# Kernel optimization log

Hardware: AMD Instinct MI355X
Metric: run time of the kernel (lower is better)

## Reference

```python
import jax, jax.numpy as jnp
import numpy as np
from jax.ops import segment_sum

N_NODES = 100000
N_EDGES = 1600000
IN_DIM, HID_DIM, OUT_DIM = 64, 48, 32


def setup_inputs() -> dict:
    key = jax.random.key(0)
    ks = jax.random.split(key, 4)
    x = jax.random.normal(ks[0], (N_NODES, IN_DIM), dtype=jnp.float32)
    edge_index = jax.random.randint(ks[1], (2, N_EDGES), 0, N_NODES, dtype=jnp.int64)
    W1 = jax.random.normal(ks[2], (IN_DIM, HID_DIM), dtype=jnp.float32) / np.sqrt(IN_DIM)
    b1 = jnp.zeros((HID_DIM,), dtype=jnp.float32)
    W2 = jax.random.normal(ks[3], (HID_DIM, OUT_DIM), dtype=jnp.float32) / np.sqrt(HID_DIM)
    b2 = jnp.zeros((OUT_DIM,), dtype=jnp.float32)
    return {"x": x, "edge_index": edge_index, "W1": W1, "b1": b1, "W2": W2, "b2": b2}


def _gcn_conv(x, W, b, src, dst, deg_inv_sqrt, n_nodes):
    # GCNConv: out = D^{-1/2} (A + I) D^{-1/2} (x W) + b
    h = x @ W                                   # [N, F_out]
    norm = deg_inv_sqrt[src] * deg_inv_sqrt[dst]  # [E+N]
    msg = h[src] * norm[:, None]                # gather + scale
    out = segment_sum(msg, dst, num_segments=n_nodes)  # scatter-add over dst
    return out + b


def reference(x, edge_index, W1, b1, W2, b2):
    n = x.shape[0]
    loop = jnp.arange(n, dtype=edge_index.dtype)
    src = jnp.concatenate([edge_index[0], loop])  # add self-loops (PyG default)
    dst = jnp.concatenate([edge_index[1], loop])
    deg = segment_sum(jnp.ones_like(dst, dtype=x.dtype), dst, num_segments=n)
    deg_inv_sqrt = jnp.where(deg > 0, jax.lax.rsqrt(jnp.maximum(deg, 1.0)), 0.0)
    h = _gcn_conv(x, W1, b1, src, dst, deg_inv_sqrt, n)
    h = jax.nn.relu(h)
    embeddings = _gcn_conv(h, W2, b2, src, dst, deg_inv_sqrt, n)
    return embeddings
```

## Files before the change

kernel.cpp:

```cpp
#include <hip/hip_runtime.h>
#include <hip/hip_fp16.h>


#define NN 100000
#define NE 1600000
#define NPB 128
#define NBUCK ((NN + NPB - 1) / NPB)
#define PBITS 17
#define PMASK ((1 << PBITS) - 1)
#define CHB 3
#define CHS 14
#define NKEY (NPB << CHB)
#define CAP 4096
#define UN 8
#define PART_B 512
#define EPT 8
#define RUNW (PART_B * EPT)
#define PART_G ((NE + RUNW - 1) / RUNW)
#define GROWS 256
#define GEMM_G ((NN + GROWS - 1) / GROWS)
#define GB NBUCK

struct alignas(8)  half4 { __half2 lo, hi; };
struct alignas(16) half8 { __half2 a, b, c, d; };

__global__ __launch_bounds__(512) void
k_lsortgemm(const int* __restrict__ src, const int* __restrict__ dst,
            int* __restrict__ runs, unsigned int* __restrict__ seg,
            const float* __restrict__ X, const float* __restrict__ W1,
            __half* __restrict__ Hh) {
    __shared__ int h[NBUCK];
    __shared__ int tsum[512];
    __shared__ int stage[RUNW];
    __shared__ float w[64 * 48];
    int tid = threadIdx.x;

    if (blockIdx.x < PART_G) {
        for (int i = tid; i < NBUCK; i += PART_B) h[i] = 0;
        __syncthreads();
        int ebase = blockIdx.x * RUNW;
        int pw[EPT], pb[EPT];
#pragma unroll
        for (int k = 0; k < EPT; ++k) {
            int e = ebase + k * PART_B + tid;
            if (e < NE) {
                int d = dst[e];
                pb[k] = d >> 7;
                pw[k] = src[e] | ((d & (NPB - 1)) << PBITS);
                atomicAdd(&h[pb[k]], 1);
            } else pb[k] = -1;
        }
        __syncthreads();
        int c0 = 0, c1 = 0;
        if (tid < NBUCK / 2) { c0 = h[2 * tid]; c1 = h[2 * tid + 1]; }
        int loc = c0 + c1;
        tsum[tid] = (tid < NBUCK / 2) ? loc : 0;
        __syncthreads();
        for (int off = 1; off < 512; off <<= 1) {
            int v = (tid >= off) ? tsum[tid - off] : 0;
            __syncthreads();
            tsum[tid] += v;
            __syncthreads();
        }
        if (tid < NBUCK / 2) {
            int base = tsum[tid] - loc;
            seg[(size_t)blockIdx.x * NBUCK + 2 * tid]     = ((unsigned)base << 9) | (unsigned)c0;
            seg[(size_t)blockIdx.x * NBUCK + 2 * tid + 1] = ((unsigned)(base + c0) << 9) | (unsigned)c1;
            h[2 * tid]     = base;
            h[2 * tid + 1] = base + c0;
        }
        __syncthreads();
#pragma unroll
        for (int k = 0; k < EPT; ++k) {
            if (pb[k] >= 0) {
                int r = atomicAdd(&h[pb[k]], 1);
                stage[r] = pw[k];
            }
        }
        __syncthreads();
#pragma unroll
        for (int k = 0; k < EPT; ++k)
            runs[(size_t)blockIdx.x * RUNW + k * PART_B + tid] = stage[k * PART_B + tid];
        return;
    }

    constexpr int NC = 48, CPT = 12, CG = 4, KF4 = 16;
    int R0 = (blockIdx.x - PART_G) * GROWS;
    for (int i = tid; i < 64 * 48; i += 512) w[i] = W1[i];
    __syncthreads();

    int tc = tid % CG, tr = tid / CG;
    int r0 = R0 + 2 * tr, r1 = r0 + 1;
    int c0 = tc * CPT;
    bool ok0 = r0 < NN, ok1 = r1 < NN;
    const float4* X4 = (const float4*)X;
    const float4 z4 = make_float4(0.f, 0.f, 0.f, 0.f);

    float acc[2][CPT];
#pragma unroll
    for (int rr = 0; rr < 2; ++rr)
#pragma unroll
        for (int j = 0; j < CPT; ++j) acc[rr][j] = 0.f;

#pragma unroll 2
    for (int k4 = 0; k4 < KF4; ++k4) {
        float4 xa = ok0 ? X4[(size_t)r0 * KF4 + k4] : z4;
        float4 xb = ok1 ? X4[(size_t)r1 * KF4 + k4] : z4;
        float ar[4] = {xa.x, xa.y, xa.z, xa.w};
        float br[4] = {xb.x, xb.y, xb.z, xb.w};
#pragma unroll
        for (int j = 0; j < 4; ++j) {
            float va = ar[j], vb = br[j];
#pragma unroll
            for (int q = 0; q < CPT / 4; ++q) {
                float4 wv = *(const float4*)&w[(4 * k4 + j) * NC + c0 + 4 * q];
                acc[0][q*4+0] = fmaf(va, wv.x, acc[0][q*4+0]);
                acc[0][q*4+1] = fmaf(va, wv.y, acc[0][q*4+1]);
                acc[0][q*4+2] = fmaf(va, wv.z, acc[0][q*4+2]);
                acc[0][q*4+3] = fmaf(va, wv.w, acc[0][q*4+3]);
                acc[1][q*4+0] = fmaf(vb, wv.x, acc[1][q*4+0]);
                acc[1][q*4+1] = fmaf(vb, wv.y, acc[1][q*4+1]);
                acc[1][q*4+2] = fmaf(vb, wv.z, acc[1][q*4+2]);
                acc[1][q*4+3] = fmaf(vb, wv.w, acc[1][q*4+3]);
            }
        }
    }
#pragma unroll
    for (int rr = 0; rr < 2; ++rr) {
        int gr = r0 + rr;
        if (gr >= NN) continue;
#pragma unroll
        for (int q = 0; q < CPT / 4; ++q) {
            __half2 p0 = __floats2half2_rn(acc[rr][q*4+0], acc[rr][q*4+1]);
            __half2 p1 = __floats2half2_rn(acc[rr][q*4+2], acc[rr][q*4+3]);
            half4 hv; hv.lo = p0; hv.hi = p1;
            *(half4*)(Hh + (size_t)gr * NC + c0 + 4 * q) = hv;
        }
    }
}

__global__ __launch_bounds__(256) void
k_bsort2(const int* __restrict__ runs, const unsigned int* __restrict__ seg,
         int* __restrict__ srcsort, unsigned int* __restrict__ rowinfo,
         float* __restrict__ dinv) {
    __shared__ int stage[CAP];
    __shared__ int cnt[NKEY];
    __shared__ int tsum[256];
    int tid = threadIdx.x, b = blockIdx.x;

    unsigned int s0 = (tid < PART_G) ? seg[(size_t)tid * NBUCK + b] : 0u;
    unsigned int s1 = (tid + 256 < PART_G) ? seg[(size_t)(tid + 256) * NBUCK + b] : 0u;
    int l0 = (int)(s0 & 511u), l1 = (int)(s1 & 511u);
    int mylen = l0 + l1;
    tsum[tid] = mylen;
    __syncthreads();
    for (int off = 1; off < 256; off <<= 1) {
        int v = (tid >= off) ? tsum[tid - off] : 0;
        __syncthreads();
        tsum[tid] += v;
        __syncthreads();
    }
    int wbase = tsum[tid] - mylen;
    int sz = tsum[255];
    {
        const int* p = runs + (size_t)tid * RUNW + (s0 >> 9);
        for (int i = 0; i < l0; ++i) stage[wbase + i] = p[i];
        p = runs + (size_t)(tid + 256) * RUNW + (s1 >> 9);
        for (int i = 0; i < l1; ++i) stage[wbase + l0 + i] = p[i];
    }
    for (int i = tid; i < NKEY; i += 256) cnt[i] = 0;
    __syncthreads();

    for (int i = tid; i < sz; i += 256) {
        int w = stage[i];
        int key = ((w >> PBITS) << CHB) | ((w & PMASK) >> CHS);
        atomicAdd(&cnt[key], 1);
    }
    __syncthreads();
    int k0 = tid * 4;
    int c0 = cnt[k0], c1 = cnt[k0 + 1], c2 = cnt[k0 + 2], c3 = cnt[k0 + 3];
    int loc = c0 + c1 + c2 + c3;
    tsum[tid] = loc;
    __syncthreads();
    for (int off = 1; off < 256; off <<= 1) {
        int v = (tid >= off) ? tsum[tid - off] : 0;
        __syncthreads();
        tsum[tid] += v;
        __syncthreads();
    }
    int base = tsum[tid] - loc;
    cnt[k0]     = base;
    cnt[k0 + 1] = base + c0;
    cnt[k0 + 2] = base + c0 + c1;
    cnt[k0 + 3] = base + c0 + c1 + c2;
    __syncthreads();
    int e0 = b * CAP;
    if (tid < NPB) {
        int node = b * NPB + tid;
        int rs = cnt[tid << CHB];
        int re = (tid == NPB - 1) ? sz : cnt[(tid + 1) << CHB];
        if (node < NN) {
            rowinfo[node] = ((unsigned int)(e0 + rs) << 10) | (unsigned int)(re - rs);
            dinv[node] = rsqrtf((float)(re - rs + 1));
        }
    }
    __syncthreads();
    for (int i = tid; i < sz; i += 256) {
        int w = stage[i];
        int key = ((w >> PBITS) << CHB) | ((w & PMASK) >> CHS);
        int p = atomicAdd(&cnt[key], 1);
        srcsort[e0 + p] = w & PMASK;
    }
}

__global__ __launch_bounds__(256) void
k_fused48(const __half* __restrict__ Hh, const unsigned int* __restrict__ rowinfo,
          const int* __restrict__ srcsort, const float* __restrict__ dinv,
          const float* __restrict__ b1, const float* __restrict__ W2,
          __half* __restrict__ Hh2) {
    constexpr int ROWS = 128, XS = 49;
    __shared__ float Xs[ROWS * XS];
    __shared__ float w2[48 * 32];
    __shared__ float bb[48];
    int tid = threadIdx.x;
    int R0 = blockIdx.x * ROWS;
    for (int i = tid; i < 48 * 32; i += 256) w2[i] = W2[i];
    if (tid < 48) bb[tid] = b1[tid];
    __syncthreads();

    for (int t = tid; t < ROWS * 6; t += 256) {
        int lr = t / 6, q = t - lr * 6;
        int r = R0 + lr;
        if (r >= NN) continue;
        float dself = dinv[r];
        half8 sv = *(const half8*)(Hh + (size_t)r * 48 + 8 * q);
        float2 f0 = __half22float2(sv.a), f1 = __half22float2(sv.b);
        float2 f2 = __half22float2(sv.c), f3 = __half22float2(sv.d);
        float a0 = f0.x * dself, a1 = f0.y * dself;
        float a2 = f1.x * dself, a3 = f1.y * dself;
        float a4 = f2.x * dself, a5 = f2.y * dself;
        float a6 = f3.x * dself, a7 = f3.y * dself;
        unsigned int rp = rowinfo[r];
        int e0 = rp >> 10, e1 = e0 + (int)(rp & 1023);
        for (int e = e0; e < e1; e += UN) {
            int ss[UN]; float ms[UN];
#pragma unroll
            for (int u = 0; u < UN; ++u) {
                int ee = e + u;
                bool ok = ee < e1;
                ss[u] = srcsort[ok ? ee : e0];
                ms[u] = ok ? 1.f : 0.f;
            }
            half8 vv[UN]; float dv[UN];
#pragma unroll
            for (int u = 0; u < UN; ++u) {
                vv[u] = *(const half8*)(Hh + (size_t)ss[u] * 48 + 8 * q);
                dv[u] = dinv[ss[u]];
            }
#pragma unroll
            for (int u = 0; u < UN; ++u) {
                float2 g0 = __half22float2(vv[u].a), g1 = __half22float2(vv[u].b);
                float2 g2 = __half22float2(vv[u].c), g3 = __half22float2(vv[u].d);
                float m = ms[u] * dv[u];
                a0 = fmaf(g0.x, m, a0); a1 = fmaf(g0.y, m, a1);
                a2 = fmaf(g1.x, m, a2); a3 = fmaf(g1.y, m, a3);
                a4 = fmaf(g2.x, m, a4); a5 = fmaf(g2.y, m, a5);
                a6 = fmaf(g3.x, m, a6); a7 = fmaf(g3.y, m, a7);
            }
        }
        float d = dself;
        float* xr = &Xs[lr * XS + 8 * q];
        const float* bf = &bb[8 * q];
        xr[0] = fmaxf(fmaf(a0, d, bf[0]), 0.f);
        xr[1] = fmaxf(fmaf(a1, d, bf[1]), 0.f);
        xr[2] = fmaxf(fmaf(a2, d, bf[2]), 0.f);
        xr[3] = fmaxf(fmaf(a3, d, bf[3]), 0.f);
        xr[4] = fmaxf(fmaf(a4, d, bf[4]), 0.f);
        xr[5] = fmaxf(fmaf(a5, d, bf[5]), 0.f);
        xr[6] = fmaxf(fmaf(a6, d, bf[6]), 0.f);
        xr[7] = fmaxf(fmaf(a7, d, bf[7]), 0.f);
    }
    __syncthreads();

    int tc = tid & 3, tr = tid >> 2;
    int r0l = 2 * tr, c0 = tc * 8;
    float acc[2][8];
#pragma unroll
    for (int rr = 0; rr < 2; ++rr)
#pragma unroll
        for (int j = 0; j < 8; ++j) acc[rr][j] = 0.f;
#pragma unroll 4
    for (int k = 0; k < 48; ++k) {
        float x0 = Xs[r0l * XS + k];
        float x1 = Xs[(r0l + 1) * XS + k];
        float4 wv0 = *(const float4*)&w2[k * 32 + c0];
        float4 wv1 = *(const float4*)&w2[k * 32 + c0 + 4];
        acc[0][0] = fmaf(x0, wv0.x, acc[0][0]); acc[0][1] = fmaf(x0, wv0.y, acc[0][1]);
        acc[0][2] = fmaf(x0, wv0.z, acc[0][2]); acc[0][3] = fmaf(x0, wv0.w, acc[0][3]);
        acc[0][4] = fmaf(x0, wv1.x, acc[0][4]); acc[0][5] = fmaf(x0, wv1.y, acc[0][5]);
        acc[0][6] = fmaf(x0, wv1.z, acc[0][6]); acc[0][7] = fmaf(x0, wv1.w, acc[0][7]);
        acc[1][0] = fmaf(x1, wv0.x, acc[1][0]); acc[1][1] = fmaf(x1, wv0.y, acc[1][1]);
        acc[1][2] = fmaf(x1, wv0.z, acc[1][2]); acc[1][3] = fmaf(x1, wv0.w, acc[1][3]);
        acc[1][4] = fmaf(x1, wv1.x, acc[1][4]); acc[1][5] = fmaf(x1, wv1.y, acc[1][5]);
        acc[1][6] = fmaf(x1, wv1.z, acc[1][6]); acc[1][7] = fmaf(x1, wv1.w, acc[1][7]);
    }
#pragma unroll
    for (int rr = 0; rr < 2; ++rr) {
        int gr = R0 + r0l + rr;
        if (gr >= NN) continue;
        float d = dinv[gr];
        __half2 p0 = __floats2half2_rn(acc[rr][0] * d, acc[rr][1] * d);
        __half2 p1 = __floats2half2_rn(acc[rr][2] * d, acc[rr][3] * d);
        __half2 p2 = __floats2half2_rn(acc[rr][4] * d, acc[rr][5] * d);
        __half2 p3 = __floats2half2_rn(acc[rr][6] * d, acc[rr][7] * d);
        half8 hv; hv.a = p0; hv.b = p1; hv.c = p2; hv.d = p3;
        *(half8*)(Hh2 + (size_t)gr * 32 + c0) = hv;
    }
}

template <int NC>
__global__ void k_agg(const __half* __restrict__ Hh, const unsigned int* __restrict__ rowinfo,
                      const int* __restrict__ srcsort, const float* __restrict__ dinv,
                      const float* __restrict__ bias, float* __restrict__ out) {
    constexpr int Q = NC / 8;
    int idx = blockIdx.x * blockDim.x + threadIdx.x;
    if (idx >= NN * Q) return;
    int r = idx / Q, q = idx - r * Q;
    half8 sv = *(const half8*)(Hh + (size_t)r * NC + 8 * q);
    float2 f0 = __half22float2(sv.a), f1 = __half22float2(sv.b);
    float2 f2 = __half22float2(sv.c), f3 = __half22float2(sv.d);
    float a0 = f0.x, a1 = f0.y, a2 = f1.x, a3 = f1.y;
    float a4 = f2.x, a5 = f2.y, a6 = f3.x, a7 = f3.y;
    unsigned int rp = rowinfo[r];
    int e0 = rp >> 10, e1 = e0 + (int)(rp & 1023);
    for (int e = e0; e < e1; e += UN) {
        int ss[UN]; float ms[UN];
#pragma unroll
        for (int u = 0; u < UN; ++u) {
            int ee = e + u;
            bool ok = ee < e1;
            ss[u] = srcsort[ok ? ee : e0];
            ms[u] = ok ? 1.f : 0.f;
        }
        half8 vv[UN];
#pragma unroll
        for (int u = 0; u < UN; ++u)
            vv[u] = *(const half8*)(Hh + (size_t)ss[u] * NC + 8 * q);
#pragma unroll
        for (int u = 0; u < UN; ++u) {
            float2 g0 = __half22float2(vv[u].a), g1 = __half22float2(vv[u].b);
            float2 g2 = __half22float2(vv[u].c), g3 = __half22float2(vv[u].d);
            float m = ms[u];
            a0 = fmaf(g0.x, m, a0); a1 = fmaf(g0.y, m, a1);
            a2 = fmaf(g1.x, m, a2); a3 = fmaf(g1.y, m, a3);
            a4 = fmaf(g2.x, m, a4); a5 = fmaf(g2.y, m, a5);
            a6 = fmaf(g3.x, m, a6); a7 = fmaf(g3.y, m, a7);
        }
    }
    float d = dinv[r];
    const float4* b4 = (const float4*)bias;
    float4 bv0 = b4[2 * q], bv1 = b4[2 * q + 1];
    a0 = fmaf(a0, d, bv0.x); a1 = fmaf(a1, d, bv0.y);
    a2 = fmaf(a2, d, bv0.z); a3 = fmaf(a3, d, bv0.w);
    a4 = fmaf(a4, d, bv1.x); a5 = fmaf(a5, d, bv1.y);
    a6 = fmaf(a6, d, bv1.z); a7 = fmaf(a7, d, bv1.w);
    float4* o4 = (float4*)(out + (size_t)r * NC + 8 * q);
    o4[0] = make_float4(a0, a1, a2, a3);
    o4[1] = make_float4(a4, a5, a6, a7);
}

extern "C" void kernel_launch(void* const* d_in, const int* in_sizes, int n_in,
                              void* d_out, int out_size, void* d_ws, size_t ws_size,
                              hipStream_t stream) {
    const float* x  = (const float*)d_in[0];
    const int*   ei = (const int*)d_in[1];
    const float* W1 = (const float*)d_in[2];
    const float* b1 = (const float*)d_in[3];
    const float* W2 = (const float*)d_in[4];
    const float* b2 = (const float*)d_in[5];
    float* out = (float*)d_out;

    const int* src = ei;
    const int* dst = ei + NE;

    char* p = (char*)d_ws;
    auto take = [&](size_t elems) { void* q = p; p += ((elems * 4 + 255) & ~255ull); return q; };
    unsigned int* rowinfo = (unsigned int*)take(NN);
    float*        dinv    = (float*)take(NN);
    int*          srcsort = (int*)take((size_t)NBUCK * CAP);
    __half*       Hh      = (__half*)take((size_t)NN * 24);
    unsigned int* seg     = (unsigned int*)take((size_t)PART_G * NBUCK);
    int*          runs    = (int*)take((size_t)PART_G * RUNW);
    __half*       Hh2     = (__half*)runs;

    const int B = 256;
    k_lsortgemm<<<PART_G + GEMM_G, PART_B, 0, stream>>>(src, dst, runs, seg, x, W1, Hh);
    k_bsort2<<<NBUCK, 256, 0, stream>>>(runs, seg, srcsort, rowinfo, dinv);
    k_fused48<<<GB, 256, 0, stream>>>(Hh, rowinfo, srcsort, dinv, b1, W2, Hh2);
    k_agg<32><<<(NN * 4 + B - 1) / B, B, 0, stream>>>(Hh2, rowinfo, srcsort, dinv, b2, out);
}
```

Before: 200.5 us.

## Prescale layer-1 features by source degree norm and move GEMM into sort kernel

The partition kernel now also counts in-degrees with global atomics, and the X·W1 GEMM moves from the partition kernel into the bucket-sort kernel, sharing LDS through a union. The GEMM output is scaled by each source node's deg^-1/2 before being stored in half precision. This removes the per-edge dinv gather from the layer-1 aggregation loop. In exchange it adds a memset, 1.6M global atomics on deg, and a changed kernel split whose load balance differs.

Result: slower. 251.8 us (+25.6%).

```diff
diff --git a/kernel.cpp b/kernel.cpp
--- a/kernel.cpp
+++ b/kernel.cpp
@@ -17,76 +17,158 @@
 #define EPT 8
 #define RUNW (PART_B * EPT)
 #define PART_G ((NE + RUNW - 1) / RUNW)
-#define GROWS 256
-#define GEMM_G ((NN + GROWS - 1) / GROWS)
 #define GB NBUCK
+#define GEMM2_G ((NN + 127) / 128)
 
 struct alignas(8)  half4 { __half2 lo, hi; };
 struct alignas(16) half8 { __half2 a, b, c, d; };
 
 __global__ __launch_bounds__(512) void
-k_lsortgemm(const int* __restrict__ src, const int* __restrict__ dst,
-            int* __restrict__ runs, unsigned int* __restrict__ seg,
-            const float* __restrict__ X, const float* __restrict__ W1,
-            __half* __restrict__ Hh) {
+k_part(const int* __restrict__ src, const int* __restrict__ dst,
+       int* __restrict__ runs, unsigned int* __restrict__ seg,
+       int* __restrict__ deg) {
     __shared__ int h[NBUCK];
     __shared__ int tsum[512];
     __shared__ int stage[RUNW];
-    __shared__ float w[64 * 48];
     int tid = threadIdx.x;
 
-    if (blockIdx.x < PART_G) {
-        for (int i = tid; i < NBUCK; i += PART_B) h[i] = 0;
-        __syncthreads();
-        int ebase = blockIdx.x * RUNW;
-        int pw[EPT], pb[EPT];
-#pragma unroll
-        for (int k = 0; k < EPT; ++k) {
-            int e = ebase + k * PART_B + tid;
-            if (e < NE) {
-                int d = dst[e];
-                pb[k] = d >> 7;
-                pw[k] = src[e] | ((d & (NPB - 1)) << PBITS);
-                atomicAdd(&h[pb[k]], 1);
-            } else pb[k] = -1;
-        }
-        __syncthreads();
-        int c0 = 0, c1 = 0;
-        if (tid < NBUCK / 2) { c0 = h[2 * tid]; c1 = h[2 * tid + 1]; }
-        int loc = c0 + c1;
-        tsum[tid] = (tid < NBUCK / 2) ? loc : 0;
-        __syncthreads();
-        for (int off = 1; off < 512; off <<= 1) {
-            int v = (tid >= off) ? tsum[tid - off] : 0;
+    for (int i = tid; i < NBUCK; i += PART_B) h[i] = 0;
+    __syncthreads();
+    int ebase = blockIdx.x * RUNW;
+    int pw[EPT], pb[EPT];
+#pragma unroll
+    for (int k = 0; k < EPT; ++k) {
+        int e = ebase + k * PART_B + tid;
+        if (e < NE) {
+            int d = dst[e];
+            pb[k] = d >> 7;
+            pw[k] = src[e] | ((d & (NPB - 1)) << PBITS);
+            atomicAdd(&h[pb[k]], 1);
+            atomicAdd(&deg[d], 1);
+        } else pb[k] = -1;
+    }
+    __syncthreads();
+    int c0 = 0, c1 = 0;
+    if (tid < NBUCK / 2) { c0 = h[2 * tid]; c1 = h[2 * tid + 1]; }
+    int loc = c0 + c1;
+    tsum[tid] = (tid < NBUCK / 2) ? loc : 0;
+    __syncthreads();
+    for (int off = 1; off < 512; off <<= 1) {
+        int v = (tid >= off) ? tsum[tid - off] : 0;
+        __syncthreads();
+        tsum[tid] += v;
+        __syncthreads();
+    }
+    if (tid < NBUCK / 2) {
+        int base = tsum[tid] - loc;
+        seg[(size_t)blockIdx.x * NBUCK + 2 * tid]     = ((unsigned)base << 9) | (unsigned)c0;
+        seg[(size_t)blockIdx.x * NBUCK + 2 * tid + 1] = ((unsigned)(base + c0) << 9) | (unsigned)c1;
+        h[2 * tid]     = base;
+        h[2 * tid + 1] = base + c0;
+    }
+    __syncthreads();
+#pragma unroll
+    for (int k = 0; k < EPT; ++k) {
+        if (pb[k] >= 0) {
+            int r = atomicAdd(&h[pb[k]], 1);
+            stage[r] = pw[k];
+        }
+    }
+    __syncthreads();
+#pragma unroll
+    for (int k = 0; k < EPT; ++k)
+        runs[(size_t)blockIdx.x * RUNW + k * PART_B + tid] = stage[k * PART_B + tid];
+}
+
+struct SortLds {
+    int stage[CAP];
+    int cnt[NKEY];
+    int tsum[256];
+};
+struct GemmLds { float w[64 * 48]; };
+union BGLds { SortLds s; GemmLds g; };
+
+__global__ __launch_bounds__(256) void
+k_bsortgemm(const int* __restrict__ runs, const unsigned int* __restrict__ seg,
+            int* __restrict__ srcsort, unsigned int* __restrict__ rowinfo,
+            float* __restrict__ dinv, const int* __restrict__ deg,
+            const float* __restrict__ X, const float* __restrict__ W1,
+            __half* __restrict__ Hh) {
+    __shared__ BGLds U;
+    int tid = threadIdx.x;
+
+    if (blockIdx.x < NBUCK) {
+        int b = blockIdx.x;
+        unsigned int s0 = (tid < PART_G) ? seg[(size_t)tid * NBUCK + b] : 0u;
+        unsigned int s1 = (tid + 256 < PART_G) ? seg[(size_t)(tid + 256) * NBUCK + b] : 0u;
+        int l0 = (int)(s0 & 511u), l1 = (int)(s1 & 511u);
+        int mylen = l0 + l1;
+        U.s.tsum[tid] = mylen;
+        __syncthreads();
+        for (int off = 1; off < 256; off <<= 1) {
+            int v = (tid >= off) ? U.s.tsum[tid - off] : 0;
             __syncthreads();
-            tsum[tid] += v;
+            U.s.tsum[tid] += v;
             __syncthreads();
         }
-        if (tid < NBUCK / 2) {
-            int base = tsum[tid] - loc;
-            seg[(size_t)blockIdx.x * NBUCK + 2 * tid]     = ((unsigned)base << 9) | (unsigned)c0;
-            seg[(size_t)blockIdx.x * NBUCK + 2 * tid + 1] = ((unsigned)(base + c0) << 9) | (unsigned)c1;
-            h[2 * tid]     = base;
-            h[2 * tid + 1] = base + c0;
-        }
-        __syncthreads();
-#pragma unroll
-        for (int k = 0; k < EPT; ++k) {
-            if (pb[k] >= 0) {
-                int r = atomicAdd(&h[pb[k]], 1);
-                stage[r] = pw[k];
+        int wbase = U.s.tsum[tid] - mylen;
+        int sz = U.s.tsum[255];
+        {
+            const int* p = runs + (size_t)tid * RUNW + (s0 >> 9);
+            for (int i = 0; i < l0; ++i) U.s.stage[wbase + i] = p[i];
+            p = runs + (size_t)(tid + 256) * RUNW + (s1 >> 9);
+            for (int i = 0; i < l1; ++i) U.s.stage[wbase + l0 + i] = p[i];
+        }
+        for (int i = tid; i < NKEY; i += 256) U.s.cnt[i] = 0;
+        __syncthreads();
+
+        for (int i = tid; i < sz; i += 256) {
+            int w = U.s.stage[i];
+            int key = ((w >> PBITS) << CHB) | ((w & PMASK) >> CHS);
+            atomicAdd(&U.s.cnt[key], 1);
+        }
+        __syncthreads();
+        int k0 = tid * 4;
+        int c0 = U.s.cnt[k0], c1 = U.s.cnt[k0 + 1];
+        int c2 = U.s.cnt[k0 + 2], c3 = U.s.cnt[k0 + 3];
+        int loc = c0 + c1 + c2 + c3;
+        U.s.tsum[tid] = loc;
+        __syncthreads();
+        for (int off = 1; off < 256; off <<= 1) {
+            int v = (tid >= off) ? U.s.tsum[tid - off] : 0;
+            __syncthreads();
+            U.s.tsum[tid] += v;
+            __syncthreads();
+        }
+        int base = U.s.tsum[tid] - loc;
+        U.s.cnt[k0]     = base;
+        U.s.cnt[k0 + 1] = base + c0;
+        U.s.cnt[k0 + 2] = base + c0 + c1;
+        U.s.cnt[k0 + 3] = base + c0 + c1 + c2;
+        __syncthreads();
+        int e0 = b * CAP;
+        if (tid < NPB) {
+            int node = b * NPB + tid;
+            int rs = U.s.cnt[tid << CHB];
+            int re = (tid == NPB - 1) ? sz : U.s.cnt[(tid + 1) << CHB];
+            if (node < NN) {
+                rowinfo[node] = ((unsigned int)(e0 + rs) << 10) | (unsigned int)(re - rs);
+                dinv[node] = rsqrtf((float)(re - rs + 1));
             }
         }
         __syncthreads();
-#pragma unroll
-        for (int k = 0; k < EPT; ++k)
-            runs[(size_t)blockIdx.x * RUNW + k * PART_B + tid] = stage[k * PART_B + tid];
+        for (int i = tid; i < sz; i += 256) {
+            int w = U.s.stage[i];
+            int key = ((w >> PBITS) << CHB) | ((w & PMASK) >> CHS);
+            int p = atomicAdd(&U.s.cnt[key], 1);
+            srcsort[e0 + p] = w & PMASK;
+        }
         return;
     }
 
     constexpr int NC = 48, CPT = 12, CG = 4, KF4 = 16;
-    int R0 = (blockIdx.x - PART_G) * GROWS;
-    for (int i = tid; i < 64 * 48; i += 512) w[i] = W1[i];
+    int R0 = (blockIdx.x - NBUCK) * 128;
+    for (int i = tid; i < 64 * 48; i += 256) U.g.w[i] = W1[i];
     __syncthreads();
 
     int tc = tid % CG, tr = tid / CG;
@@ -113,7 +195,7 @@
             float va = ar[j], vb = br[j];
 #pragma unroll
             for (int q = 0; q < CPT / 4; ++q) {
-                float4 wv = *(const float4*)&w[(4 * k4 + j) * NC + c0 + 4 * q];
+                float4 wv = *(const float4*)&U.g.w[(4 * k4 + j) * NC + c0 + 4 * q];
                 acc[0][q*4+0] = fmaf(va, wv.x, acc[0][q*4+0]);
                 acc[0][q*4+1] = fmaf(va, wv.y, acc[0][q*4+1]);
                 acc[0][q*4+2] = fmaf(va, wv.z, acc[0][q*4+2]);
@@ -129,87 +211,14 @@
     for (int rr = 0; rr < 2; ++rr) {
         int gr = r0 + rr;
         if (gr >= NN) continue;
+        float d = rsqrtf((float)deg[gr] + 1.0f);
 #pragma unroll
         for (int q = 0; q < CPT / 4; ++q) {
-            __half2 p0 = __floats2half2_rn(acc[rr][q*4+0], acc[rr][q*4+1]);
-            __half2 p1 = __floats2half2_rn(acc[rr][q*4+2], acc[rr][q*4+3]);
+            __half2 p0 = __floats2half2_rn(acc[rr][q*4+0] * d, acc[rr][q*4+1] * d);
+            __half2 p1 = __floats2half2_rn(acc[rr][q*4+2] * d, acc[rr][q*4+3] * d);
             half4 hv; hv.lo = p0; hv.hi = p1;
             *(half4*)(Hh + (size_t)gr * NC + c0 + 4 * q) = hv;
         }
-    }
-}
-
-__global__ __launch_bounds__(256) void
-k_bsort2(const int* __restrict__ runs, const unsigned int* __restrict__ seg,
-         int* __restrict__ srcsort, unsigned int* __restrict__ rowinfo,
-         float* __restrict__ dinv) {
-    __shared__ int stage[CAP];
-    __shared__ int cnt[NKEY];
-    __shared__ int tsum[256];
-    int tid = threadIdx.x, b = blockIdx.x;
-
-    unsigned int s0 = (tid < PART_G) ? seg[(size_t)tid * NBUCK + b] : 0u;
-    unsigned int s1 = (tid + 256 < PART_G) ? seg[(size_t)(tid + 256) * NBUCK + b] : 0u;
-    int l0 = (int)(s0 & 511u), l1 = (int)(s1 & 511u);
-    int mylen = l0 + l1;
-    tsum[tid] = mylen;
-    __syncthreads();
-    for (int off = 1; off < 256; off <<= 1) {
-        int v = (tid >= off) ? tsum[tid - off] : 0;
-        __syncthreads();
-        tsum[tid] += v;
-        __syncthreads();
-    }
-    int wbase = tsum[tid] - mylen;
-    int sz = tsum[255];
-    {
-        const int* p = runs + (size_t)tid * RUNW + (s0 >> 9);
-        for (int i = 0; i < l0; ++i) stage[wbase + i] = p[i];
-        p = runs + (size_t)(tid + 256) * RUNW + (s1 >> 9);
-        for (int i = 0; i < l1; ++i) stage[wbase + l0 + i] = p[i];
-    }
-    for (int i = tid; i < NKEY; i += 256) cnt[i] = 0;
-    __syncthreads();
-
-    for (int i = tid; i < sz; i += 256) {
-        int w = stage[i];
-        int key = ((w >> PBITS) << CHB) | ((w & PMASK) >> CHS);
-        atomicAdd(&cnt[key], 1);
-    }
-    __syncthreads();
-    int k0 = tid * 4;
-    int c0 = cnt[k0], c1 = cnt[k0 + 1], c2 = cnt[k0 + 2], c3 = cnt[k0 + 3];
-    int loc = c0 + c1 + c2 + c3;
-    tsum[tid] = loc;
-    __syncthreads();
-    for (int off = 1; off < 256; off <<= 1) {
-        int v = (tid >= off) ? tsum[tid - off] : 0;
-        __syncthreads();
-        tsum[tid] += v;
-        __syncthreads();
-    }
-    int base = tsum[tid] - loc;
-    cnt[k0]     = base;
-    cnt[k0 + 1] = base + c0;
-    cnt[k0 + 2] = base + c0 + c1;
-    cnt[k0 + 3] = base + c0 + c1 + c2;
-    __syncthreads();
-    int e0 = b * CAP;
-    if (tid < NPB) {
-        int node = b * NPB + tid;
-        int rs = cnt[tid << CHB];
-        int re = (tid == NPB - 1) ? sz : cnt[(tid + 1) << CHB];
-        if (node < NN) {
-            rowinfo[node] = ((unsigned int)(e0 + rs) << 10) | (unsigned int)(re - rs);
-            dinv[node] = rsqrtf((float)(re - rs + 1));
-        }
-    }
-    __syncthreads();
-    for (int i = tid; i < sz; i += 256) {
-        int w = stage[i];
-        int key = ((w >> PBITS) << CHB) | ((w & PMASK) >> CHS);
-        int p = atomicAdd(&cnt[key], 1);
-        srcsort[e0 + p] = w & PMASK;
     }
 }
 
@@ -232,14 +241,11 @@
         int lr = t / 6, q = t - lr * 6;
         int r = R0 + lr;
         if (r >= NN) continue;
-        float dself = dinv[r];
         half8 sv = *(const half8*)(Hh + (size_t)r * 48 + 8 * q);
         float2 f0 = __half22float2(sv.a), f1 = __half22float2(sv.b);
         float2 f2 = __half22float2(sv.c), f3 = __half22float2(sv.d);
-        float a0 = f0.x * dself, a1 = f0.y * dself;
-        float a2 = f1.x * dself, a3 = f1.y * dself;
-        float a4 = f2.x * dself, a5 = f2.y * dself;
-        float a6 = f3.x * dself, a7 = f3.y * dself;
+        float a0 = f0.x, a1 = f0.y, a2 = f1.x, a3 = f1.y;
+        float a4 = f2.x, a5 = f2.y, a6 = f3.x, a7 = f3.y;
         unsigned int rp = rowinfo[r];
         int e0 = rp >> 10, e1 = e0 + (int)(rp & 1023);
         for (int e = e0; e < e1; e += UN) {
@@ -251,24 +257,22 @@
                 ss[u] = srcsort[ok ? ee : e0];
                 ms[u] = ok ? 1.f : 0.f;
             }
-            half8 vv[UN]; float dv[UN];
-#pragma unroll
-            for (int u = 0; u < UN; ++u) {
+            half8 vv[UN];
+#pragma unroll
+            for (int u = 0; u < UN; ++u)
                 vv[u] = *(const half8*)(Hh + (size_t)ss[u] * 48 + 8 * q);
-                dv[u] = dinv[ss[u]];
-            }
 #pragma unroll
             for (int u = 0; u < UN; ++u) {
                 float2 g0 = __half22float2(vv[u].a), g1 = __half22float2(vv[u].b);
                 float2 g2 = __half22float2(vv[u].c), g3 = __half22float2(vv[u].d);
-                float m = ms[u] * dv[u];
+                float m = ms[u];
                 a0 = fmaf(g0.x, m, a0); a1 = fmaf(g0.y, m, a1);
                 a2 = fmaf(g1.x, m, a2); a3 = fmaf(g1.y, m, a3);
                 a4 = fmaf(g2.x, m, a4); a5 = fmaf(g2.y, m, a5);
                 a6 = fmaf(g3.x, m, a6); a7 = fmaf(g3.y, m, a7);
             }
         }
-        float d = dself;
+        float d = dinv[r];
         float* xr = &Xs[lr * XS + 8 * q];
         const float* bf = &bb[8 * q];
         xr[0] = fmaxf(fmaf(a0, d, bf[0]), 0.f);
@@ -387,6 +391,7 @@
     auto take = [&](size_t elems) { void* q = p; p += ((elems * 4 + 255) & ~255ull); return q; };
     unsigned int* rowinfo = (unsigned int*)take(NN);
     float*        dinv    = (float*)take(NN);
+    int*          deg     = (int*)take(NN);
     int*          srcsort = (int*)take((size_t)NBUCK * CAP);
     __half*       Hh      = (__half*)take((size_t)NN * 24);
     unsigned int* seg     = (unsigned int*)take((size_t)PART_G * NBUCK);
@@ -394,8 +399,10 @@
     __half*       Hh2     = (__half*)runs;
 
     const int B = 256;
-    k_lsortgemm<<<PART_G + GEMM_G, PART_B, 0, stream>>>(src, dst, runs, seg, x, W1, Hh);
-    k_bsort2<<<NBUCK, 256, 0, stream>>>(runs, seg, srcsort, rowinfo, dinv);
+    hipMemsetAsync(deg, 0, NN * sizeof(int), stream);
+    k_part<<<PART_G, PART_B, 0, stream>>>(src, dst, runs, seg, deg);
+    k_bsortgemm<<<NBUCK + GEMM2_G, 256, 0, stream>>>(runs, seg, srcsort, rowinfo,
+                                                     dinv, deg, x, W1, Hh);
     k_fused48<<<GB, 256, 0, stream>>>(Hh, rowinfo, srcsort, dinv, b1, W2, Hh2);
     k_agg<32><<<(NN * 4 + B - 1) / B, B, 0, stream>>>(Hh2, rowinfo, srcsort, dinv, b2, out);
 }
```
